# Performance work log

Measured on AMD Instinct MI355X. Metric: run time of the kernel, lower is better.

The kernel has to match this reference:

```python
import jax, jax.numpy as jnp
import numpy as np

D_MODEL = 1024
NHEAD = 16
HEAD_DIM = D_MODEL // NHEAD
MAX_SEQ = 512


def _rope_tables(seq_len):
    dim_half = HEAD_DIM // 2
    pos = jnp.arange(seq_len, dtype=jnp.float32)
    freqs = 1.0 / (10000.0 ** (jnp.arange(dim_half, dtype=jnp.float32) / dim_half))
    angles = pos[:, None] * freqs[None, :]  # [S, dim_half]
    return jnp.sin(angles), jnp.cos(angles)


def setup_inputs() -> dict:
    key = jax.random.key(0)
    ks = jax.random.split(key, 5)
    x = jax.random.normal(ks[0], (8, 512, D_MODEL), dtype=jnp.float32)
    s = 1.0 / np.sqrt(D_MODEL)
    W_qkv = jax.random.uniform(ks[1], (D_MODEL, 3 * D_MODEL), jnp.float32, -s, s)
    b_qkv = jax.random.uniform(ks[2], (3 * D_MODEL,), jnp.float32, -s, s)
    W_out = jax.random.uniform(ks[3], (D_MODEL, D_MODEL), jnp.float32, -s, s)
    b_out = jax.random.uniform(ks[4], (D_MODEL,), jnp.float32, -s, s)
    return {"x": x, "W_qkv": W_qkv, "b_qkv": b_qkv, "W_out": W_out, "b_out": b_out}


def reference(x, W_qkv, b_qkv, W_out, b_out):
    B, S, _ = x.shape
    qkv = x @ W_qkv + b_qkv                                   # [B,S,3D]
    qkv = qkv.reshape(B, S, 3, NHEAD, HEAD_DIM).transpose(2, 0, 3, 1, 4)
    q, k, v = qkv[0], qkv[1], qkv[2]                          # [B,H,S,Dh]
    sin, cos = _rope_tables(S)                                # [S, Dh/2]
    dh = HEAD_DIM // 2
    q1, q2 = q[..., :dh], q[..., dh:]
    k1, k2 = k[..., :dh], k[..., dh:]
    q = jnp.concatenate([q1 * cos - q2 * sin, q1 * sin + q2 * cos], axis=-1)
    k = jnp.concatenate([k1 * cos - k2 * sin, k1 * sin + k2 * cos], axis=-1)
    scores = jnp.einsum('bhqd,bhkd->bhqk', q, k) / np.sqrt(HEAD_DIM)
    attn = jax.nn.softmax(scores, axis=-1)                    # dropout: eval mode (identity)
    out = jnp.einsum('bhqk,bhkd->bhqd', attn, v)
    out = out.transpose(0, 2, 1, 3).reshape(B, S, D_MODEL)
    return out @ W_out + b_out
```

## Files before the change

### kernel.cpp

```cpp
#include <hip/hip_runtime.h>
#include <hip/hip_bf16.h>

#define NB 8
#define SEQ 512
#define DMODEL 1024
#define NHEAD 16
#define HDIM 64
typedef __hip_bfloat16 bf16;
typedef __attribute__((ext_vector_type(8))) short short8;
typedef __attribute__((ext_vector_type(4))) float f32x4;

__device__ __forceinline__ void glds16(const void* g, void* l) {
    __builtin_amdgcn_global_load_lds(
        (const __attribute__((address_space(1))) unsigned int*)g,
        (__attribute__((address_space(3))) unsigned int*)l, 16, 0, 0);
}

__global__ __launch_bounds__(256)
void cast_bf16_k(const float* __restrict__ X, bf16* __restrict__ Xb) {
    int i = (blockIdx.x * 256 + threadIdx.x) * 8;
    float4 v0 = *(const float4*)&X[i];
    float4 v1 = *(const float4*)&X[i + 4];
    bf16 o[8];
    o[0] = __float2bfloat16(v0.x); o[1] = __float2bfloat16(v0.y);
    o[2] = __float2bfloat16(v0.z); o[3] = __float2bfloat16(v0.w);
    o[4] = __float2bfloat16(v1.x); o[5] = __float2bfloat16(v1.y);
    o[6] = __float2bfloat16(v1.z); o[7] = __float2bfloat16(v1.w);
    *(uint4*)&Xb[i] = *(uint4*)o;
}

__global__ __launch_bounds__(256)
void transpose_cast_k(const float* __restrict__ W, bf16* __restrict__ Wt,
                      int R, int C) {
    __shared__ float t[64][65];
    int k0 = blockIdx.y * 64, n0 = blockIdx.x * 64;
    int c = threadIdx.x & 63, r = threadIdx.x >> 6;
    #pragma unroll 4
    for (int i = 0; i < 16; ++i)
        t[r + i * 4][c] = W[(size_t)(k0 + r + i * 4) * C + n0 + c];
    __syncthreads();
    #pragma unroll 4
    for (int i = 0; i < 16; ++i)
        Wt[(size_t)(n0 + r + i * 4) * R + k0 + c] = __float2bfloat16(t[c][r + i * 4]);
}

#define GEMM_MAINLOOP(Agp, Bgp)                                               \
    __shared__ __align__(16) short Asm[128 * 64];                             \
    __shared__ __align__(16) short Bsm[128 * 64];                             \
    int tid = threadIdx.x;                                                    \
    int lane = tid & 63, wid = tid >> 6;                                      \
    int wr = wid >> 1, wc = wid & 1;                                          \
    int lj = lane & 15, li = lane >> 4;                                       \
    f32x4 acc[4][4] = {};                                                     \
    for (int ks = 0; ks < 16; ++ks) {                                         \
        int k0 = ks * 64;                                                     \
        int srow = (lane >> 3), ssl = lane & 7;                               \
        _Pragma("unroll")                                                     \
        for (int q = 0; q < 4; ++q) {                                         \
            int seg = wid * 4 + q;                                            \
            int row = seg * 8 + srow;                                         \
            int cg = ssl ^ (row & 7);                                         \
            glds16(Agp + ((size_t)(m0 + row) * 1024 + k0 + cg * 8),           \
                   (char*)Asm + seg * 1024);                                  \
            glds16(Bgp + ((size_t)(n0 + row) * 1024 + k0 + cg * 8),           \
                   (char*)Bsm + seg * 1024);                                  \
        }                                                                     \
        __syncthreads();                                                      \
        _Pragma("unroll")                                                     \
        for (int kk = 0; kk < 2; ++kk) {                                      \
            short8 af[4], bf[4];                                              \
            _Pragma("unroll")                                                 \
            for (int mf = 0; mf < 4; ++mf) {                                  \
                int r = wr * 64 + mf * 16 + lj;                               \
                int ck = kk * 4 + li;                                         \
                af[mf] = *(const short8*)((const char*)Asm +                  \
                          (r * 128 + ((ck ^ (r & 7)) * 16)));                 \
            }                                                                 \
            _Pragma("unroll")                                                 \
            for (int nf = 0; nf < 4; ++nf) {                                  \
                int r = wc * 64 + nf * 16 + lj;                               \
                int ck = kk * 4 + li;                                         \
                bf[nf] = *(const short8*)((const char*)Bsm +                  \
                          (r * 128 + ((ck ^ (r & 7)) * 16)));                 \
            }                                                                 \
            _Pragma("unroll")                                                 \
            for (int mf = 0; mf < 4; ++mf)                                    \
                _Pragma("unroll")                                             \
                for (int nf = 0; nf < 4; ++nf)                                \
                    acc[mf][nf] = __builtin_amdgcn_mfma_f32_16x16x32_bf16(    \
                        af[mf], bf[nf], acc[mf][nf], 0, 0, 0);                \
        }                                                                     \
        __syncthreads();                                                      \
    }

__global__ __launch_bounds__(256)
void qkv_mfma_k(const bf16* __restrict__ Xb, const bf16* __restrict__ Wt,
                const float* __restrict__ bias,
                bf16* __restrict__ Qb, bf16* __restrict__ Kb, bf16* __restrict__ Vt) {
    int m0 = blockIdx.y * 128, n0 = blockIdx.x * 128;
    GEMM_MAINLOOP(Xb, Wt)
    int ncol = n0 + wc * 64;
    int c = ncol >> 10;
    int h = (ncol & 1023) >> 6;
    #pragma unroll
    for (int nf = 0; nf < 2; ++nf) {
        int p = nf * 16 + lj;
        float b1 = bias[ncol + p], b2 = bias[ncol + p + 32];
        float freq = __expf(-(float)p * 0.28782313662425574f);
        #pragma unroll
        for (int mf = 0; mf < 4; ++mf) {
            #pragma unroll
            for (int j = 0; j < 4; ++j) {
                int m = m0 + wr * 64 + mf * 16 + li * 4 + j;
                int bb = m >> 9, s = m & 511;
                float v1 = acc[mf][nf][j] + b1;
                float v2 = acc[mf][nf + 2][j] + b2;
                if (c == 2) {
                    size_t tb = (size_t)(bb * NHEAD + h) * HDIM;
                    Vt[(tb + p) * SEQ + s]      = __float2bfloat16(v1);
                    Vt[(tb + p + 32) * SEQ + s] = __float2bfloat16(v2);
                } else {
                    float sv, cv;
                    sincosf((float)s * freq, &sv, &cv);
                    float o1 = v1 * cv - v2 * sv;
                    float o2 = v1 * sv + v2 * cv;
                    bf16* dst = (c == 0) ? Qb : Kb;
                    size_t base = ((size_t)(bb * NHEAD + h) * SEQ + s) * HDIM;
                    dst[base + p]      = __float2bfloat16(o1);
                    dst[base + p + 32] = __float2bfloat16(o2);
                }
            }
        }
    }
}

__global__ __launch_bounds__(256)
void out_mfma_k(const bf16* __restrict__ Ab, const bf16* __restrict__ Wt,
                const float* __restrict__ bias, float* __restrict__ out) {
    int m0 = blockIdx.y * 128, n0 = blockIdx.x * 128;
    GEMM_MAINLOOP(Ab, Wt)
    int col0 = n0 + wc * 64;
    #pragma unroll
    for (int nf = 0; nf < 4; ++nf) {
        int col = col0 + nf * 16 + lj;
        float bv = bias[col];
        #pragma unroll
        for (int mf = 0; mf < 4; ++mf)
            #pragma unroll
            for (int j = 0; j < 4; ++j) {
                int m = m0 + wr * 64 + mf * 16 + li * 4 + j;
                out[(size_t)m * DMODEL + col] = acc[mf][nf][j] + bv;
            }
    }
}

__global__ __launch_bounds__(256)
void attn_mfma_k(const bf16* __restrict__ Qb, const bf16* __restrict__ Kb,
                 const bf16* __restrict__ Vt, bf16* __restrict__ Ab) {
    __shared__ __align__(16) short Qsm[64 * 64];
    __shared__ __align__(16) short Ksm[64 * 64];
    __shared__ __align__(16) short Vsm[64 * 64];
    __shared__ __align__(16) short Psm[64 * 64];
    int tid = threadIdx.x;
    int lane = tid & 63, wid = tid >> 6;
    int lj = lane & 15, li = lane >> 4;
    int bh = blockIdx.x >> 3, qt = blockIdx.x & 7;
    const bf16* Qp = Qb + ((size_t)bh * SEQ + qt * 64) * HDIM;
    const bf16* Kp = Kb + (size_t)bh * SEQ * HDIM;
    const bf16* Vp = Vt + (size_t)bh * HDIM * SEQ;
    int srow = lane >> 3, ssl = lane & 7;
    #pragma unroll
    for (int q = 0; q < 2; ++q) {
        int seg = wid * 2 + q;
        int row = seg * 8 + srow;
        int cg = ssl ^ (row & 7);
        glds16(Qp + ((size_t)row * 64 + cg * 8), (char*)Qsm + seg * 1024);
    }
    float m_[4], l_[4];
    f32x4 acc_o[4] = {};
    #pragma unroll
    for (int j = 0; j < 4; ++j) { m_[j] = -1e30f; l_[j] = 0.f; }
    __syncthreads();
    for (int kt = 0; kt < 8; ++kt) {
        #pragma unroll
        for (int q = 0; q < 2; ++q) {
            int seg = wid * 2 + q;
            int row = seg * 8 + srow;
            int cg = ssl ^ (row & 7);
            glds16(Kp + ((size_t)(kt * 64 + row) * 64 + cg * 8),
                   (char*)Ksm + seg * 1024);
            glds16(Vp + ((size_t)row * SEQ + kt * 64 + cg * 8),
                   (char*)Vsm + seg * 1024);
        }
        __syncthreads();
        f32x4 sacc[4] = {};
        #pragma unroll
        for (int kk = 0; kk < 2; ++kk) {
            int r = wid * 16 + lj;
            int ck = kk * 4 + li;
            short8 af = *(const short8*)((const char*)Qsm +
                         (r * 128 + ((ck ^ (r & 7)) * 16)));
            #pragma unroll
            for (int nf = 0; nf < 4; ++nf) {
                int rb = nf * 16 + lj;
                short8 kf = *(const short8*)((const char*)Ksm +
                             (rb * 128 + ((ck ^ (rb & 7)) * 16)));
                sacc[nf] = __builtin_amdgcn_mfma_f32_16x16x32_bf16(af, kf, sacc[nf], 0, 0, 0);
            }
        }
        float p[4][4];
        #pragma unroll
        for (int j = 0; j < 4; ++j) {
            float s0 = sacc[0][j] * 0.125f, s1 = sacc[1][j] * 0.125f;
            float s2 = sacc[2][j] * 0.125f, s3 = sacc[3][j] * 0.125f;
            float tm = fmaxf(fmaxf(s0, s1), fmaxf(s2, s3));
            tm = fmaxf(tm, __shfl_xor(tm, 1));
            tm = fmaxf(tm, __shfl_xor(tm, 2));
            tm = fmaxf(tm, __shfl_xor(tm, 4));
            tm = fmaxf(tm, __shfl_xor(tm, 8));
            float mn = fmaxf(m_[j], tm);
            float sc = __expf(m_[j] - mn);
            p[0][j] = __expf(s0 - mn); p[1][j] = __expf(s1 - mn);
            p[2][j] = __expf(s2 - mn); p[3][j] = __expf(s3 - mn);
            float ts = p[0][j] + p[1][j] + p[2][j] + p[3][j];
            ts += __shfl_xor(ts, 1); ts += __shfl_xor(ts, 2);
            ts += __shfl_xor(ts, 4); ts += __shfl_xor(ts, 8);
            l_[j] = l_[j] * sc + ts;
            m_[j] = mn;
            acc_o[0][j] *= sc; acc_o[1][j] *= sc;
            acc_o[2][j] *= sc; acc_o[3][j] *= sc;
        }
        #pragma unroll
        for (int nf = 0; nf < 4; ++nf)
            #pragma unroll
            for (int j = 0; j < 4; ++j) {
                int row = wid * 16 + li * 4 + j;
                int col = nf * 16 + lj;
                int cl = col >> 3;
                *(bf16*)((char*)Psm + row * 128 + ((cl ^ (row & 7)) * 16) +
                         (col & 7) * 2) = __float2bfloat16(p[nf][j]);
            }
        #pragma unroll
        for (int kk = 0; kk < 2; ++kk) {
            int r = wid * 16 + lj;
            int ck = kk * 4 + li;
            short8 pa = *(const short8*)((const char*)Psm +
                         (r * 128 + ((ck ^ (r & 7)) * 16)));
            #pragma unroll
            for (int nf = 0; nf < 4; ++nf) {
                int rb = nf * 16 + lj;
                short8 vf = *(const short8*)((const char*)Vsm +
                             (rb * 128 + ((ck ^ (rb & 7)) * 16)));
                acc_o[nf] = __builtin_amdgcn_mfma_f32_16x16x32_bf16(pa, vf, acc_o[nf], 0, 0, 0);
            }
        }
        __syncthreads();
    }
    int b = bh >> 4, h = bh & 15;
    #pragma unroll
    for (int j = 0; j < 4; ++j) {
        float inv = 1.0f / l_[j];
        int s = qt * 64 + wid * 16 + li * 4 + j;
        #pragma unroll
        for (int nf = 0; nf < 4; ++nf) {
            int d = nf * 16 + lj;
            Ab[((size_t)b * SEQ + s) * DMODEL + h * 64 + d] =
                __float2bfloat16(acc_o[nf][j] * inv);
        }
    }
}

extern "C" void kernel_launch(void* const* d_in, const int* in_sizes, int n_in,
                              void* d_out, int out_size, void* d_ws, size_t ws_size,
                              hipStream_t stream) {
    const float *x = nullptr, *Wqkv = nullptr, *bqkv = nullptr,
                *Wout = nullptr, *bout = nullptr;
    for (int i = 0; i < n_in; ++i) {
        switch (in_sizes[i]) {
            case NB * SEQ * DMODEL:   x    = (const float*)d_in[i]; break;
            case DMODEL * 3 * DMODEL: Wqkv = (const float*)d_in[i]; break;
            case 3 * DMODEL:          bqkv = (const float*)d_in[i]; break;
            case DMODEL * DMODEL:     Wout = (const float*)d_in[i]; break;
            case DMODEL:              bout = (const float*)d_in[i]; break;
        }
    }
    if (!x)    x    = (const float*)d_in[0];
    if (!Wqkv) Wqkv = (const float*)d_in[1];
    if (!bqkv) bqkv = (const float*)d_in[2];
    if (!Wout) Wout = (const float*)d_in[3];
    if (!bout) bout = (const float*)d_in[4];
    float* out = (float*)d_out;

    char* ws = (char*)d_ws;
    bf16* Xb     = (bf16*)(ws);
    bf16* Ab     = (bf16*)(ws);
    bf16* Wqkv_t = (bf16*)(ws + 8388608);
    bf16* Wout_t = (bf16*)(ws + 14680064);
    bf16* Qb     = (bf16*)(ws + 16777216);
    bf16* Kb     = (bf16*)(ws + 25165824);
    bf16* Vt     = (bf16*)(ws + 33554432);

    cast_bf16_k<<<2048, 256, 0, stream>>>(x, Xb);
    transpose_cast_k<<<dim3(48, 16), 256, 0, stream>>>(Wqkv, Wqkv_t, DMODEL, 3 * DMODEL);
    transpose_cast_k<<<dim3(16, 16), 256, 0, stream>>>(Wout, Wout_t, DMODEL, DMODEL);
    qkv_mfma_k<<<dim3(24, 32), 256, 0, stream>>>(Xb, Wqkv_t, bqkv, Qb, Kb, Vt);
    attn_mfma_k<<<NB * NHEAD * 8, 256, 0, stream>>>(Qb, Kb, Vt, Ab);
    out_mfma_k<<<dim3(8, 32), 256, 0, stream>>>(Ab, Wout_t, bout, out);
}
```

Measured before the change: 202.2 us.

## Double-buffer LDS tiles in GEMM and attention kernels to overlap loads

Converts the shared GEMM main loop and the attention K/V loop to double-buffered LDS. The next k-tile (or K/V tile) is issued via global_load_lds before computing on the current buffer, and the barrier after issuing loads is removed. This aims to hide global-to-LDS latency behind MFMA work. In exchange it doubles LDS per block (64KB for GEMM), which can lower blocks per CU, and it depends on the end-of-iteration barrier waiting for the async loads.

```diff
diff --git a/kernel.cpp b/kernel.cpp
--- a/kernel.cpp
+++ b/kernel.cpp
@@ -44,43 +44,56 @@
         Wt[(size_t)(n0 + r + i * 4) * R + k0 + c] = __float2bfloat16(t[c][r + i * 4]);
 }
 
-#define GEMM_MAINLOOP(Agp, Bgp)                                               \
-    __shared__ __align__(16) short Asm[128 * 64];                             \
-    __shared__ __align__(16) short Bsm[128 * 64];                             \
+#define GEMM_MAINLOOP_DB(Agp, Bgp)                                            \
+    __shared__ __align__(16) short Asm[2][128 * 64];                          \
+    __shared__ __align__(16) short Bsm[2][128 * 64];                          \
     int tid = threadIdx.x;                                                    \
     int lane = tid & 63, wid = tid >> 6;                                      \
     int wr = wid >> 1, wc = wid & 1;                                          \
     int lj = lane & 15, li = lane >> 4;                                       \
+    int srow = lane >> 3, ssl = lane & 7;                                     \
     f32x4 acc[4][4] = {};                                                     \
+    _Pragma("unroll")                                                         \
+    for (int q = 0; q < 4; ++q) {                                             \
+        int seg = wid * 4 + q;                                                \
+        int row = seg * 8 + srow;                                             \
+        int cg = ssl ^ (row & 7);                                             \
+        glds16(Agp + ((size_t)(m0 + row) * 1024 + cg * 8),                    \
+               (char*)Asm[0] + seg * 1024);                                   \
+        glds16(Bgp + ((size_t)(n0 + row) * 1024 + cg * 8),                    \
+               (char*)Bsm[0] + seg * 1024);                                   \
+    }                                                                         \
+    __syncthreads();                                                          \
     for (int ks = 0; ks < 16; ++ks) {                                         \
-        int k0 = ks * 64;                                                     \
-        int srow = (lane >> 3), ssl = lane & 7;                               \
-        _Pragma("unroll")                                                     \
-        for (int q = 0; q < 4; ++q) {                                         \
-            int seg = wid * 4 + q;                                            \
-            int row = seg * 8 + srow;                                         \
-            int cg = ssl ^ (row & 7);                                         \
-            glds16(Agp + ((size_t)(m0 + row) * 1024 + k0 + cg * 8),           \
-                   (char*)Asm + seg * 1024);                                  \
-            glds16(Bgp + ((size_t)(n0 + row) * 1024 + k0 + cg * 8),           \
-                   (char*)Bsm + seg * 1024);                                  \
+        int cur = ks & 1;                                                     \
+        if (ks + 1 < 16) {                                                    \
+            int k0 = (ks + 1) * 64;                                           \
+            _Pragma("unroll")                                                 \
+            for (int q = 0; q < 4; ++q) {                                     \
+                int seg = wid * 4 + q;                                        \
+                int row = seg * 8 + srow;                                     \
+                int cg = ssl ^ (row & 7);                                     \
+                glds16(Agp + ((size_t)(m0 + row) * 1024 + k0 + cg * 8),       \
+                       (char*)Asm[cur ^ 1] + seg * 1024);                     \
+                glds16(Bgp + ((size_t)(n0 + row) * 1024 + k0 + cg * 8),       \
+                       (char*)Bsm[cur ^ 1] + seg * 1024);                     \
+            }                                                                 \
         }                                                                     \
-        __syncthreads();                                                      \
         _Pragma("unroll")                                                     \
         for (int kk = 0; kk < 2; ++kk) {                                      \
-            short8 af[4], bf[4];                                              \
+            short8 af[4], bfr[4];                                             \
             _Pragma("unroll")                                                 \
             for (int mf = 0; mf < 4; ++mf) {                                  \
                 int r = wr * 64 + mf * 16 + lj;                               \
                 int ck = kk * 4 + li;                                         \
-                af[mf] = *(const short8*)((const char*)Asm +                  \
+                af[mf] = *(const short8*)((const char*)Asm[cur] +             \
                           (r * 128 + ((ck ^ (r & 7)) * 16)));                 \
             }                                                                 \
             _Pragma("unroll")                                                 \
             for (int nf = 0; nf < 4; ++nf) {                                  \
                 int r = wc * 64 + nf * 16 + lj;                               \
                 int ck = kk * 4 + li;                                         \
-                bf[nf] = *(const short8*)((const char*)Bsm +                  \
+                bfr[nf] = *(const short8*)((const char*)Bsm[cur] +            \
                           (r * 128 + ((ck ^ (r & 7)) * 16)));                 \
             }                                                                 \
             _Pragma("unroll")                                                 \
@@ -88,7 +101,7 @@
                 _Pragma("unroll")                                             \
                 for (int nf = 0; nf < 4; ++nf)                                \
                     acc[mf][nf] = __builtin_amdgcn_mfma_f32_16x16x32_bf16(    \
-                        af[mf], bf[nf], acc[mf][nf], 0, 0, 0);                \
+                        af[mf], bfr[nf], acc[mf][nf], 0, 0, 0);               \
         }                                                                     \
         __syncthreads();                                                      \
     }
@@ -98,7 +111,7 @@
                 const float* __restrict__ bias,
                 bf16* __restrict__ Qb, bf16* __restrict__ Kb, bf16* __restrict__ Vt) {
     int m0 = blockIdx.y * 128, n0 = blockIdx.x * 128;
-    GEMM_MAINLOOP(Xb, Wt)
+    GEMM_MAINLOOP_DB(Xb, Wt)
     int ncol = n0 + wc * 64;
     int c = ncol >> 10;
     int h = (ncol & 1023) >> 6;
@@ -138,7 +151,7 @@
 void out_mfma_k(const bf16* __restrict__ Ab, const bf16* __restrict__ Wt,
                 const float* __restrict__ bias, float* __restrict__ out) {
     int m0 = blockIdx.y * 128, n0 = blockIdx.x * 128;
-    GEMM_MAINLOOP(Ab, Wt)
+    GEMM_MAINLOOP_DB(Ab, Wt)
     int col0 = n0 + wc * 64;
     #pragma unroll
     for (int nf = 0; nf < 4; ++nf) {
@@ -158,8 +171,8 @@
 void attn_mfma_k(const bf16* __restrict__ Qb, const bf16* __restrict__ Kb,
                  const bf16* __restrict__ Vt, bf16* __restrict__ Ab) {
     __shared__ __align__(16) short Qsm[64 * 64];
-    __shared__ __align__(16) short Ksm[64 * 64];
-    __shared__ __align__(16) short Vsm[64 * 64];
+    __shared__ __align__(16) short Ksm[2][64 * 64];
+    __shared__ __align__(16) short Vsm[2][64 * 64];
     __shared__ __align__(16) short Psm[64 * 64];
     int tid = threadIdx.x;
     int lane = tid & 63, wid = tid >> 6;
@@ -175,6 +188,8 @@
         int row = seg * 8 + srow;
         int cg = ssl ^ (row & 7);
         glds16(Qp + ((size_t)row * 64 + cg * 8), (char*)Qsm + seg * 1024);
+        glds16(Kp + ((size_t)row * 64 + cg * 8), (char*)Ksm[0] + seg * 1024);
+        glds16(Vp + ((size_t)row * SEQ + cg * 8), (char*)Vsm[0] + seg * 1024);
     }
     float m_[4], l_[4];
     f32x4 acc_o[4] = {};
@@ -182,17 +197,19 @@
     for (int j = 0; j < 4; ++j) { m_[j] = -1e30f; l_[j] = 0.f; }
     __syncthreads();
     for (int kt = 0; kt < 8; ++kt) {
-        #pragma unroll
-        for (int q = 0; q < 2; ++q) {
-            int seg = wid * 2 + q;
-            int row = seg * 8 + srow;
-            int cg = ssl ^ (row & 7);
-            glds16(Kp + ((size_t)(kt * 64 + row) * 64 + cg * 8),
-                   (char*)Ksm + seg * 1024);
-            glds16(Vp + ((size_t)row * SEQ + kt * 64 + cg * 8),
-                   (char*)Vsm + seg * 1024);
-        }
-        __syncthreads();
+        int cur = kt & 1;
+        if (kt + 1 < 8) {
+            #pragma unroll
+            for (int q = 0; q < 2; ++q) {
+                int seg = wid * 2 + q;
+                int row = seg * 8 + srow;
+                int cg = ssl ^ (row & 7);
+                glds16(Kp + ((size_t)((kt + 1) * 64 + row) * 64 + cg * 8),
+                       (char*)Ksm[cur ^ 1] + seg * 1024);
+                glds16(Vp + ((size_t)row * SEQ + (kt + 1) * 64 + cg * 8),
+                       (char*)Vsm[cur ^ 1] + seg * 1024);
+            }
+        }
         f32x4 sacc[4] = {};
         #pragma unroll
         for (int kk = 0; kk < 2; ++kk) {
@@ -203,7 +220,7 @@
             #pragma unroll
             for (int nf = 0; nf < 4; ++nf) {
                 int rb = nf * 16 + lj;
-                short8 kf = *(const short8*)((const char*)Ksm +
+                short8 kf = *(const short8*)((const char*)Ksm[cur] +
                              (rb * 128 + ((ck ^ (rb & 7)) * 16)));
                 sacc[nf] = __builtin_amdgcn_mfma_f32_16x16x32_bf16(af, kf, sacc[nf], 0, 0, 0);
             }
@@ -249,7 +266,7 @@
             #pragma unroll
             for (int nf = 0; nf < 4; ++nf) {
                 int rb = nf * 16 + lj;
-                short8 vf = *(const short8*)((const char*)Vsm +
+                short8 vf = *(const short8*)((const char*)Vsm[cur] +
                              (rb * 128 + ((ck ^ (rb & 7)) * 16)));
                 acc_o[nf] = __builtin_amdgcn_mfma_f32_16x16x32_bf16(pa, vf, acc_o[nf], 0, 0, 0);
             }
```

Measured after the change: 212.1 us. +4.9%, slower.
